# Kernel optimization log

Hardware: AMD Instinct MI355X
Metric: run time of the kernel (lower is better)

## Reference

```python
import jax, jax.numpy as jnp
import numpy as np

VOCAB, EMBED, UNITS = 32000, 512, 1024
B, T = 32, 128


def setup_inputs() -> dict:
    key = jax.random.key(0)
    ks = jax.random.split(key, 8)
    g = lambda k, shape, s: jax.random.normal(k, shape, jnp.float32) * s
    return {
        "tokens": jax.random.randint(ks[0], (B, T), 0, VOCAB),
        "emb_table": g(ks[1], (VOCAB, EMBED), 0.02),
        "kernel_f": g(ks[2], (EMBED, 3 * UNITS), 0.02),
        "rec_kernel_f": g(ks[3], (UNITS, 3 * UNITS), 0.02),
        "bias_f": g(ks[4], (2, 3 * UNITS), 0.02),
        "kernel_b": g(ks[5], (EMBED, 3 * UNITS), 0.02),
        "rec_kernel_b": g(ks[6], (UNITS, 3 * UNITS), 0.02),
        "bias_b": g(ks[7], (2, 3 * UNITS), 0.02),
    }


def _gru(x, kernel, rec_kernel, bias, reverse):
    # Keras GRU, reset_after=True. x: [B,T,E] -> outputs [B,T,U], final state [B,U]
    units = rec_kernel.shape[0]
    x_proj = jnp.einsum('bte,eu->btu', x, kernel) + bias[0]  # input-side gates, all timesteps
    xp = jnp.swapaxes(x_proj, 0, 1)  # [T,B,3U] for scan
    h0 = jnp.zeros((x.shape[0], units), x.dtype)

    def step(h, xpt):
        rec = h @ rec_kernel + bias[1]
        xz, xr, xh = jnp.split(xpt, 3, axis=-1)
        rz, rr, rh = jnp.split(rec, 3, axis=-1)
        z = jax.nn.sigmoid(xz + rz)          # update gate
        r = jax.nn.sigmoid(xr + rr)          # reset gate
        hh = jnp.tanh(xh + r * rh)           # candidate (reset applied after recurrent matmul)
        hn = z * h + (1.0 - z) * hh
        return hn, hn

    hT, ys = jax.lax.scan(step, h0, xp, reverse=reverse)
    return jnp.swapaxes(ys, 0, 1), hT  # outputs back to [B,T,U]


def reference(tokens, emb_table, kernel_f, rec_kernel_f, bias_f, kernel_b, rec_kernel_b, bias_b):
    x = emb_table[tokens]  # [B,T,E]
    yf, hf = _gru(x, kernel_f, rec_kernel_f, bias_f, reverse=False)
    yb, hb = _gru(x, kernel_b, rec_kernel_b, bias_b, reverse=True)  # Bidirectional backward dir
    return yf + yb, hf, hb  # merge_mode='sum', states [h_forward, h_backward]
```

## Files before the change

### kernel.cpp

```cpp
#include <hip/hip_runtime.h>


using u16 = unsigned short;
using u32 = unsigned int;
typedef __attribute__((ext_vector_type(8))) short bfx8;
typedef __attribute__((ext_vector_type(4))) float f32x4;
typedef __attribute__((ext_vector_type(4))) u32 u32x4;
typedef __attribute__((ext_vector_type(4))) u16 u16x4;

#define B_ 32
#define T_ 128
#define E_ 512
#define U_ 1024
#define NG 3072
#define M_ 4096
#define YN 4194304
#define ROTB 131072
#define HXD  393216

__device__ __forceinline__ float bf2f(u16 u) {
  union { u32 i; float f; } v; v.i = (u32)u << 16; return v.f;
}
__device__ __forceinline__ u16 f2bf(float f) {
  union { float f; u32 i; } v; v.f = f;
  u32 r = v.i + 0x7FFFu + ((v.i >> 16) & 1u);
  return (u16)(r >> 16);
}
__device__ __forceinline__ float sigm(float x) { return 1.0f / (1.0f + __expf(-x)); }
__device__ __forceinline__ float ftanh(float x) {
  float e = __expf(2.f * x);
  return 1.f - 2.f / (e + 1.f);
}

__device__ __forceinline__ void load_lds16(const void* g, void* l) {
  __builtin_amdgcn_global_load_lds(
      (const __attribute__((address_space(1))) u32*)g,
      (__attribute__((address_space(3))) u32*)l, 16, 0, 0);
}

__global__ __launch_bounds__(256) void k_embed(const int* __restrict__ tok,
                                               const float* __restrict__ emb,
                                               u16* __restrict__ X) {
  int idx = blockIdx.x * 256 + threadIdx.x;
  int m = idx >> 6, k8 = (idx & 63) << 3;
  int b = m & 31, t = m >> 5;
  int tk = tok[b * T_ + t];
  const float* s = emb + (size_t)tk * E_ + k8;
  float4 v0 = *(const float4*)s, v1 = *(const float4*)(s + 4);
  bfx8 r;
  r[0]=(short)f2bf(v0.x); r[1]=(short)f2bf(v0.y); r[2]=(short)f2bf(v0.z); r[3]=(short)f2bf(v0.w);
  r[4]=(short)f2bf(v1.x); r[5]=(short)f2bf(v1.y); r[6]=(short)f2bf(v1.z); r[7]=(short)f2bf(v1.w);
  *(bfx8*)(X + (size_t)m * E_ + k8) = r;
}

__global__ void k_transpose(const float* __restrict__ in, u16* __restrict__ out,
                            int K, int N, int remap) {
  __shared__ float tile[32][33];
  int k0 = blockIdx.x * 32, n0 = blockIdx.y * 32;
  int tx = threadIdx.x, ty = threadIdx.y;
  for (int j = ty; j < 32; j += 8) tile[j][tx] = in[(size_t)(k0 + j) * N + n0 + tx];
  __syncthreads();
  for (int j = ty; j < 32; j += 8) {
    int n = n0 + j;
    int row = remap ? ((((n & 1023) >> 5) * 96) + ((n >> 10) << 5) + (n & 31)) : n;
    out[(size_t)row * K + k0 + tx] = f2bf(tile[tx][j]);
  }
}

__global__ __launch_bounds__(256) void k_xproj(const u16* __restrict__ X,
                                               const u16* __restrict__ WT,
                                               const float* __restrict__ biasF,
                                               const float* __restrict__ biasB,
                                               u16* __restrict__ XP) {
  const int n0 = blockIdx.x * 128, m0 = blockIdx.y * 128, dir = blockIdx.z;
  const float* bias = dir ? biasB : biasF;
  const u16* Wd = WT + (size_t)dir * NG * E_;
  __shared__ __align__(16) u16 As[128 * 64];
  __shared__ __align__(16) u16 Bs[128 * 64];
  const int tid = threadIdx.x;
  const int wave = tid >> 6, lane = tid & 63;
  const int moff = (wave >> 1) * 64, noff = (wave & 1) * 64;
  const int l15 = lane & 15, l4 = lane >> 4;
  f32x4 acc[4][4] = {};
  for (int kt = 0; kt < 8; ++kt) {
    int k0 = kt * 64;
#pragma unroll
    for (int j = 0; j < 4; ++j) {
      int o = j * 4096 + tid * 16;
      int row = o >> 7;
      int kk = (((o & 127) ^ ((row & 7) << 4)) >> 1);
      load_lds16(X  + (size_t)(m0 + row) * E_ + k0 + kk, (char*)As + o);
      load_lds16(Wd + (size_t)(n0 + row) * E_ + k0 + kk, (char*)Bs + o);
    }
    __syncthreads();
#pragma unroll
    for (int Ks = 0; Ks < 2; ++Ks) {
      bfx8 a[4], b[4];
#pragma unroll
      for (int Mt = 0; Mt < 4; ++Mt) {
        int ra = moff + Mt * 16 + l15;
        int ba = (ra << 7) + ((Ks * 32 + l4 * 8) << 1);
        ba ^= (ra & 7) << 4;
        a[Mt] = *(const bfx8*)((const char*)As + ba);
      }
#pragma unroll
      for (int Nt = 0; Nt < 4; ++Nt) {
        int rb = noff + Nt * 16 + l15;
        int bb2 = (rb << 7) + ((Ks * 32 + l4 * 8) << 1);
        bb2 ^= (rb & 7) << 4;
        b[Nt] = *(const bfx8*)((const char*)Bs + bb2);
      }
#pragma unroll
      for (int Mt = 0; Mt < 4; ++Mt)
#pragma unroll
        for (int Nt = 0; Nt < 4; ++Nt)
          acc[Mt][Nt] = __builtin_amdgcn_mfma_f32_16x16x32_bf16(a[Mt], b[Nt], acc[Mt][Nt], 0, 0, 0);
    }
    __syncthreads();
  }
  float bv[4];
#pragma unroll
  for (int Nt = 0; Nt < 4; ++Nt) bv[Nt] = bias[n0 + noff + Nt * 16 + l15];
#pragma unroll
  for (int Mt = 0; Mt < 4; ++Mt)
#pragma unroll
    for (int Nt = 0; Nt < 4; ++Nt)
#pragma unroll
      for (int r = 0; r < 4; ++r) {
        int m = m0 + moff + Mt * 16 + l4 * 4 + r;
        int n = n0 + noff + Nt * 16 + l15;
        XP[((size_t)dir * M_ + m) * NG + n] = f2bf(acc[Mt][Nt][r] + bv[Nt]);
      }
}

__global__ __launch_bounds__(256, 1) void k_gru(
    const u16* __restrict__ RW,
    u16* __restrict__ XP,
    const float* __restrict__ bf_, const float* __restrict__ bb_,
    char* __restrict__ Hx,
    float* __restrict__ out) {
  const int tid = threadIdx.x;
  const int wave = tid >> 6, lane = tid & 63;
  const int wg = blockIdx.x;
  const int dir = wg & 1, slice = wg >> 1;
  const int u0 = slice * 32;
  const float* b1p = (dir ? bb_ : bf_) + NG;
  const u16* wbase = RW + (size_t)dir * NG * U_ + (size_t)slice * 96 * U_;
  u16* xpd = XP + (size_t)dir * M_ * NG;
  char* hxd = Hx + (size_t)dir * HXD;
  __shared__ float pl[4][32][97];

  const int l15 = lane & 15, l4 = lane >> 4;

  bfx8 wf[6][8];
#pragma unroll
  for (int Nt = 0; Nt < 6; ++Nt)
#pragma unroll
    for (int Ks = 0; Ks < 8; ++Ks) {
      int c = Nt * 16 + l15;
      int k = wave * 256 + Ks * 32 + l4 * 8;
      wf[Nt][Ks] = *(const bfx8*)(wbase + (size_t)c * U_ + k);
    }

  const int eb = tid & 31;
  const int ug = tid >> 5;
  const int uu = ug * 4;
  float b1[3][4];
#pragma unroll
  for (int g = 0; g < 3; ++g)
#pragma unroll
    for (int j = 0; j < 4; ++j) b1[g][j] = b1p[g * U_ + u0 + uu + j];
  float hreg[4] = {0.f, 0.f, 0.f, 0.f};

  const int offb = wave * 32768 + l4 * 1024 + l15 * 16;
  const int soff = (slice * 8 + ug) * 512 + eb * 16;

  u16x4 xc[3];
  {
    int t0 = dir ? 127 : 0;
    const u16* xr = xpd + (size_t)(t0 * 32 + eb) * NG + u0 + uu;
#pragma unroll
    for (int g = 0; g < 3; ++g) xc[g] = *(const u16x4*)(xr + g * U_);
  }

  int rl = 0, rs = 1;
  for (int e = 0; e < 128; ++e) {
    f32x4 acc[2][6] = {};
    u16x4 xn[3] = {xc[0], xc[1], xc[2]};
    if (e > 0) {
      const u32 etag = (u32)e;
      char* rbase = hxd + rl * ROTB;
      u32x4 L[2][8], L2[2][8];
      int guard = 0;
      while (1) {
#pragma unroll
        for (int Ks = 0; Ks < 8; ++Ks) {
          const char* a = rbase + offb + Ks * 4096;
          asm volatile("global_load_dwordx4 %0, %1, off sc0 sc1"             : "=v"(L[0][Ks])  : "v"(a));
          asm volatile("global_load_dwordx4 %0, %1, off offset:256 sc0 sc1" : "=v"(L2[0][Ks]) : "v"(a));
          asm volatile("global_load_dwordx4 %0, %1, off offset:512 sc0 sc1" : "=v"(L[1][Ks])  : "v"(a));
          asm volatile("global_load_dwordx4 %0, %1, off offset:768 sc0 sc1" : "=v"(L2[1][Ks]) : "v"(a));
        }
        asm volatile("s_waitcnt vmcnt(0)");
#pragma unroll
        for (int h = 0; h < 2; ++h)
#pragma unroll
          for (int Ks = 0; Ks < 8; ++Ks)
            asm volatile("" : "+v"(L[h][Ks]), "+v"(L2[h][Ks]));
        u32 bad = 0;
#pragma unroll
        for (int h = 0; h < 2; ++h)
#pragma unroll
          for (int Ks = 0; Ks < 8; ++Ks)
            bad |= (L[h][Ks].z ^ etag) | (L2[h][Ks].z ^ etag);
        if (__all((int)(bad == 0))) break;
        if (++guard > (1 << 18)) break;
        __builtin_amdgcn_s_sleep(1);
      }
      bfx8 af[2][8];
#pragma unroll
      for (int Ks = 0; Ks < 8; ++Ks) {
        u32x4 f0 = {L[0][Ks].x, L[0][Ks].y, L[1][Ks].x, L[1][Ks].y};
        u32x4 f1 = {L2[0][Ks].x, L2[0][Ks].y, L2[1][Ks].x, L2[1][Ks].y};
        af[0][Ks] = __builtin_bit_cast(bfx8, f0);
        af[1][Ks] = __builtin_bit_cast(bfx8, f1);
      }
      if (e < 127) {
        int tn = dir ? (126 - e) : (e + 1);
        const u16* xr = xpd + (size_t)(tn * 32 + eb) * NG + u0 + uu;
#pragma unroll
        for (int g = 0; g < 3; ++g) xn[g] = *(const u16x4*)(xr + g * U_);
      }
      __builtin_amdgcn_sched_barrier(0);
#pragma unroll
      for (int Ks = 0; Ks < 8; ++Ks)
#pragma unroll
        for (int Mt = 0; Mt < 2; ++Mt)
#pragma unroll
          for (int Nt = 0; Nt < 6; ++Nt)
            acc[Mt][Nt] = __builtin_amdgcn_mfma_f32_16x16x32_bf16(af[Mt][Ks], wf[Nt][Ks],
                                                                  acc[Mt][Nt], 0, 0, 0);
    } else {
      int tn = dir ? 126 : 1;
      const u16* xr = xpd + (size_t)(tn * 32 + eb) * NG + u0 + uu;
#pragma unroll
      for (int g = 0; g < 3; ++g) xn[g] = *(const u16x4*)(xr + g * U_);
    }
#pragma unroll
    for (int Mt = 0; Mt < 2; ++Mt)
#pragma unroll
      for (int Nt = 0; Nt < 6; ++Nt)
#pragma unroll
        for (int r = 0; r < 4; ++r)
          pl[wave][Mt * 16 + l4 * 4 + r][Nt * 16 + l15] = acc[Mt][Nt][r];
    __syncthreads();
    float hold[4];
#pragma unroll
    for (int j = 0; j < 4; ++j) hold[j] = hreg[j];
#pragma unroll
    for (int j = 0; j < 4; ++j) {
      int c = uu + j;
      float rz = pl[0][eb][c]      + pl[1][eb][c]      + pl[2][eb][c]      + pl[3][eb][c];
      float rr = pl[0][eb][32 + c] + pl[1][eb][32 + c] + pl[2][eb][32 + c] + pl[3][eb][32 + c];
      float rh = pl[0][eb][64 + c] + pl[1][eb][64 + c] + pl[2][eb][64 + c] + pl[3][eb][64 + c];
      float z  = sigm(bf2f(xc[0][j]) + rz + b1[0][j]);
      float r  = sigm(bf2f(xc[1][j]) + rr + b1[1][j]);
      float hh = ftanh(bf2f(xc[2][j]) + r * (rh + b1[2][j]));
      hreg[j] = z * hreg[j] + (1.f - z) * hh;
    }
    {
      u32 p01 = (u32)f2bf(hreg[0]) | ((u32)f2bf(hreg[1]) << 16);
      u32 p23 = (u32)f2bf(hreg[2]) | ((u32)f2bf(hreg[3]) << 16);
      u32x4 sv; sv.x = p01; sv.y = p23; sv.z = (u32)(e + 1); sv.w = (u32)(e + 1);
      char* sa = hxd + rs * ROTB + soff;
      asm volatile("global_store_dwordx4 %0, %1, off sc0 sc1" :: "v"(sa), "v"(sv));
    }
    if (e > 0) {
      const int tp = dir ? (128 - e) : (e - 1);
      float* yrow = (float*)(xpd + (size_t)(tp * 32 + eb) * NG);
      *(float4*)(yrow + u0 + uu) = make_float4(hold[0], hold[1], hold[2], hold[3]);
    }
    xc[0] = xn[0]; xc[1] = xn[1]; xc[2] = xn[2];
    rl = rs; rs = (rs == 2) ? 0 : rs + 1;
    __syncthreads();
  }
  {
    const char* pa = hxd + 2 * ROTB + ((lane & 31) * 8 + 7) * 512 + 31 * 16;
    int g = 0;
    while (1) {
      u32 tv = 128u;
      if (lane < 32) {
        u32x4 tvv;
        asm volatile("global_load_dwordx4 %0, %1, off sc0 sc1\n\ts_waitcnt vmcnt(0)"
                     : "=v"(tvv) : "v"(pa));
        tv = tvv.z;
      }
      if (__all((int)(tv == 128u))) break;
      if (++g > (1 << 22)) break;
      __builtin_amdgcn_s_sleep(1);
    }
    const int tl = dir ? 0 : 127;
    float* yrow = (float*)(xpd + (size_t)(tl * 32 + eb) * NG);
    *(float4*)(yrow + u0 + uu) = make_float4(hreg[0], hreg[1], hreg[2], hreg[3]);
    float* os = out + YN + (size_t)dir * (B_ * U_) + (size_t)eb * U_ + u0 + uu;
    *(float4*)os = make_float4(hreg[0], hreg[1], hreg[2], hreg[3]);
  }
}

__global__ __launch_bounds__(256) void k_merge(const u16* __restrict__ XP,
                                               float* __restrict__ out) {
  int idx = blockIdx.x * 256 + threadIdx.x;
  int u4 = (idx & 255) * 4;
  int m = idx >> 8;
  int t = m >> 5, b = m & 31;
  const float* yf = (const float*)(XP + (size_t)m * NG);
  const float* yb = (const float*)(XP + (size_t)(M_ + m) * NG);
  float4 a = *(const float4*)(yf + u4);
  float4 c = *(const float4*)(yb + u4);
  float4 o; o.x = a.x + c.x; o.y = a.y + c.y; o.z = a.z + c.z; o.w = a.w + c.w;
  *(float4*)(out + ((size_t)b * T_ + t) * U_ + u4) = o;
}

extern "C" void kernel_launch(void* const* d_in, const int* in_sizes, int n_in,
                              void* d_out, int out_size, void* d_ws, size_t ws_size,
                              hipStream_t stream) {
  const int*   tokens = (const int*)d_in[0];
  const float* emb    = (const float*)d_in[1];
  const float* kf     = (const float*)d_in[2];
  const float* rkf    = (const float*)d_in[3];
  const float* bf_    = (const float*)d_in[4];
  const float* kb     = (const float*)d_in[5];
  const float* rkb    = (const float*)d_in[6];
  const float* bb_    = (const float*)d_in[7];
  float* out = (float*)d_out;
  char* ws = (char*)d_ws;

  u16*  X  = (u16*)ws;
  u16*  WT = (u16*)(ws + 0x400000);
  char* Hx = ws + 0x400000;
  u16*  RW = (u16*)(ws + 0xA00000);
  u16*  XP = (u16*)(ws + 0x1600000);

  k_embed<<<1024, 256, 0, stream>>>(tokens, emb, X);
  k_transpose<<<dim3(16, 96), dim3(32, 8), 0, stream>>>(kf,  WT,               512,  NG, 0);
  k_transpose<<<dim3(16, 96), dim3(32, 8), 0, stream>>>(kb,  WT + 3072 * 512,  512,  NG, 0);
  k_transpose<<<dim3(32, 96), dim3(32, 8), 0, stream>>>(rkf, RW,               1024, NG, 1);
  k_transpose<<<dim3(32, 96), dim3(32, 8), 0, stream>>>(rkb, RW + 3072 * 1024, 1024, NG, 1);
  k_xproj<<<dim3(24, 32, 2), 256, 0, stream>>>(X, WT, bf_, bb_, XP);
  hipMemsetAsync(Hx, 0, 2 * HXD, stream);
  k_gru<<<64, 256, 0, stream>>>(RW, XP, bf_, bb_, Hx, out);
  k_merge<<<4096, 256, 0, stream>>>(XP, out);
}
```

Measured before the change: 627.0 us.

## Split GRU hidden-state poll into halves and overlap MFMA with the second half

The recurrent step now issues all hidden-state loads up front, waits only for the first half (vmcnt(16)), checks its step tags and runs the first four K-slices of MFMAs while the second half is still in flight. On a tag mismatch, each half is re-polled separately. The four weight-transpose launches are also merged into one 3D-grid kernel to cut launch overhead. This lets the per-step latency of cross-workgroup state exchange overlap with compute, at the cost of more complex polling logic and extra register pressure.

```diff
diff --git a/kernel.cpp b/kernel.cpp
--- a/kernel.cpp
+++ b/kernel.cpp
@@ -53,17 +53,22 @@
   *(bfx8*)(X + (size_t)m * E_ + k8) = r;
 }
 
-__global__ void k_transpose(const float* __restrict__ in, u16* __restrict__ out,
-                            int K, int N, int remap) {
+__global__ void k_transpose_all(const float* __restrict__ kf, const float* __restrict__ kb,
+                                const float* __restrict__ rkf, const float* __restrict__ rkb,
+                                u16* __restrict__ WT, u16* __restrict__ RW) {
   __shared__ float tile[32][33];
-  int k0 = blockIdx.x * 32, n0 = blockIdx.y * 32;
+  const int z = blockIdx.z;
+  const float* in; u16* outp; int K, remap, bx;
+  if (blockIdx.x < 16) { in = z ? kb : kf;   outp = WT + (size_t)z * 3072 * 512;  K = 512;  remap = 0; bx = blockIdx.x; }
+  else                 { in = z ? rkb : rkf; outp = RW + (size_t)z * 3072 * 1024; K = 1024; remap = 1; bx = blockIdx.x - 16; }
+  int k0 = bx * 32, n0 = blockIdx.y * 32;
   int tx = threadIdx.x, ty = threadIdx.y;
-  for (int j = ty; j < 32; j += 8) tile[j][tx] = in[(size_t)(k0 + j) * N + n0 + tx];
+  for (int j = ty; j < 32; j += 8) tile[j][tx] = in[(size_t)(k0 + j) * NG + n0 + tx];
   __syncthreads();
   for (int j = ty; j < 32; j += 8) {
     int n = n0 + j;
     int row = remap ? ((((n & 1023) >> 5) * 96) + ((n >> 10) << 5) + (n & 31)) : n;
-    out[(size_t)row * K + k0 + tx] = f2bf(tile[tx][j]);
+    outp[(size_t)row * K + k0 + tx] = f2bf(tile[tx][j]);
   }
 }
 
@@ -133,6 +138,13 @@
       }
 }
 
+#define GISS(Ks) { \
+  const char* a_ = rbase + offb + (Ks) * 4096; \
+  asm volatile("global_load_dwordx4 %0, %1, off sc0 sc1"             : "=v"(L[0][Ks])  : "v"(a_)); \
+  asm volatile("global_load_dwordx4 %0, %1, off offset:256 sc0 sc1" : "=v"(L2[0][Ks]) : "v"(a_)); \
+  asm volatile("global_load_dwordx4 %0, %1, off offset:512 sc0 sc1" : "=v"(L[1][Ks])  : "v"(a_)); \
+  asm volatile("global_load_dwordx4 %0, %1, off offset:768 sc0 sc1" : "=v"(L2[1][Ks]) : "v"(a_)); }
+
 __global__ __launch_bounds__(256, 1) void k_gru(
     const u16* __restrict__ RW,
     u16* __restrict__ XP,
@@ -191,39 +203,68 @@
       const u32 etag = (u32)e;
       char* rbase = hxd + rl * ROTB;
       u32x4 L[2][8], L2[2][8];
-      int guard = 0;
-      while (1) {
-#pragma unroll
-        for (int Ks = 0; Ks < 8; ++Ks) {
-          const char* a = rbase + offb + Ks * 4096;
-          asm volatile("global_load_dwordx4 %0, %1, off sc0 sc1"             : "=v"(L[0][Ks])  : "v"(a));
-          asm volatile("global_load_dwordx4 %0, %1, off offset:256 sc0 sc1" : "=v"(L2[0][Ks]) : "v"(a));
-          asm volatile("global_load_dwordx4 %0, %1, off offset:512 sc0 sc1" : "=v"(L[1][Ks])  : "v"(a));
-          asm volatile("global_load_dwordx4 %0, %1, off offset:768 sc0 sc1" : "=v"(L2[1][Ks]) : "v"(a));
+      GISS(0) GISS(1) GISS(2) GISS(3)
+      GISS(4) GISS(5) GISS(6) GISS(7)
+      {
+        asm volatile("s_waitcnt vmcnt(16)");
+        int guard = 0;
+        while (1) {
+          u32 bad = 0;
+#pragma unroll
+          for (int Ks = 0; Ks < 4; ++Ks) {
+            asm volatile("" : "+v"(L[0][Ks]), "+v"(L2[0][Ks]), "+v"(L[1][Ks]), "+v"(L2[1][Ks]));
+            bad |= (L[0][Ks].z ^ etag) | (L2[0][Ks].z ^ etag) |
+                   (L[1][Ks].z ^ etag) | (L2[1][Ks].z ^ etag);
+          }
+          if (__all((int)(bad == 0))) break;
+          if (++guard > (1 << 18)) break;
+          __builtin_amdgcn_s_sleep(1);
+          GISS(0) GISS(1) GISS(2) GISS(3)
+          asm volatile("s_waitcnt vmcnt(0)");
         }
-        asm volatile("s_waitcnt vmcnt(0)");
-#pragma unroll
-        for (int h = 0; h < 2; ++h)
-#pragma unroll
-          for (int Ks = 0; Ks < 8; ++Ks)
-            asm volatile("" : "+v"(L[h][Ks]), "+v"(L2[h][Ks]));
-        u32 bad = 0;
-#pragma unroll
-        for (int h = 0; h < 2; ++h)
-#pragma unroll
-          for (int Ks = 0; Ks < 8; ++Ks)
-            bad |= (L[h][Ks].z ^ etag) | (L2[h][Ks].z ^ etag);
-        if (__all((int)(bad == 0))) break;
-        if (++guard > (1 << 18)) break;
-        __builtin_amdgcn_s_sleep(1);
-      }
-      bfx8 af[2][8];
-#pragma unroll
-      for (int Ks = 0; Ks < 8; ++Ks) {
+      }
+      bfx8 afA[2][4];
+#pragma unroll
+      for (int Ks = 0; Ks < 4; ++Ks) {
         u32x4 f0 = {L[0][Ks].x, L[0][Ks].y, L[1][Ks].x, L[1][Ks].y};
         u32x4 f1 = {L2[0][Ks].x, L2[0][Ks].y, L2[1][Ks].x, L2[1][Ks].y};
-        af[0][Ks] = __builtin_bit_cast(bfx8, f0);
-        af[1][Ks] = __builtin_bit_cast(bfx8, f1);
+        afA[0][Ks] = __builtin_bit_cast(bfx8, f0);
+        afA[1][Ks] = __builtin_bit_cast(bfx8, f1);
+      }
+      __builtin_amdgcn_sched_barrier(0);
+#pragma unroll
+      for (int Ks = 0; Ks < 4; ++Ks)
+#pragma unroll
+        for (int Mt = 0; Mt < 2; ++Mt)
+#pragma unroll
+          for (int Nt = 0; Nt < 6; ++Nt)
+            acc[Mt][Nt] = __builtin_amdgcn_mfma_f32_16x16x32_bf16(afA[Mt][Ks], wf[Nt][Ks],
+                                                                  acc[Mt][Nt], 0, 0, 0);
+      {
+        asm volatile("s_waitcnt vmcnt(0)");
+        int guard = 0;
+        while (1) {
+          u32 bad = 0;
+#pragma unroll
+          for (int Ks = 4; Ks < 8; ++Ks) {
+            asm volatile("" : "+v"(L[0][Ks]), "+v"(L2[0][Ks]), "+v"(L[1][Ks]), "+v"(L2[1][Ks]));
+            bad |= (L[0][Ks].z ^ etag) | (L2[0][Ks].z ^ etag) |
+                   (L[1][Ks].z ^ etag) | (L2[1][Ks].z ^ etag);
+          }
+          if (__all((int)(bad == 0))) break;
+          if (++guard > (1 << 18)) break;
+          __builtin_amdgcn_s_sleep(1);
+          GISS(4) GISS(5) GISS(6) GISS(7)
+          asm volatile("s_waitcnt vmcnt(0)");
+        }
+      }
+      bfx8 afB[2][4];
+#pragma unroll
+      for (int Ks = 4; Ks < 8; ++Ks) {
+        u32x4 f0 = {L[0][Ks].x, L[0][Ks].y, L[1][Ks].x, L[1][Ks].y};
+        u32x4 f1 = {L2[0][Ks].x, L2[0][Ks].y, L2[1][Ks].x, L2[1][Ks].y};
+        afB[0][Ks - 4] = __builtin_bit_cast(bfx8, f0);
+        afB[1][Ks - 4] = __builtin_bit_cast(bfx8, f1);
       }
       if (e < 127) {
         int tn = dir ? (126 - e) : (e + 1);
@@ -233,12 +274,12 @@
       }
       __builtin_amdgcn_sched_barrier(0);
 #pragma unroll
-      for (int Ks = 0; Ks < 8; ++Ks)
+      for (int Ks = 0; Ks < 4; ++Ks)
 #pragma unroll
         for (int Mt = 0; Mt < 2; ++Mt)
 #pragma unroll
           for (int Nt = 0; Nt < 6; ++Nt)
-            acc[Mt][Nt] = __builtin_amdgcn_mfma_f32_16x16x32_bf16(af[Mt][Ks], wf[Nt][Ks],
+            acc[Mt][Nt] = __builtin_amdgcn_mfma_f32_16x16x32_bf16(afB[Mt][Ks], wf[Nt][Ks + 4],
                                                                   acc[Mt][Nt], 0, 0, 0);
     } else {
       int tn = dir ? 126 : 1;
@@ -342,10 +383,7 @@
   u16*  XP = (u16*)(ws + 0x1600000);
 
   k_embed<<<1024, 256, 0, stream>>>(tokens, emb, X);
-  k_transpose<<<dim3(16, 96), dim3(32, 8), 0, stream>>>(kf,  WT,               512,  NG, 0);
-  k_transpose<<<dim3(16, 96), dim3(32, 8), 0, stream>>>(kb,  WT + 3072 * 512,  512,  NG, 0);
-  k_transpose<<<dim3(32, 96), dim3(32, 8), 0, stream>>>(rkf, RW,               1024, NG, 1);
-  k_transpose<<<dim3(32, 96), dim3(32, 8), 0, stream>>>(rkb, RW + 3072 * 1024, 1024, NG, 1);
+  k_transpose_all<<<dim3(48, 96, 2), dim3(32, 8), 0, stream>>>(kf, kb, rkf, rkb, WT, RW);
   k_xproj<<<dim3(24, 32, 2), 256, 0, stream>>>(X, WT, bf_, bb_, XP);
   hipMemsetAsync(Hx, 0, 2 * HXD, stream);
   k_gru<<<64, 256, 0, stream>>>(RW, XP, bf_, bb_, Hx, out);
```

Measured after the change: 619.9 us. No clear change (-1.1%).
